# Performance work log

Hardware: AMD Instinct MI355X
Metric: run time of the kernel (lower is better)

Reference implementation:

```python
import jax, jax.numpy as jnp
import numpy as np

MEAN = jnp.array([0.4488, 0.4371, 0.404], dtype=jnp.float32)
PS, PM, PL = 1e-4, 2e-4, 3e-4  # per-branch time costs ps/pm/pl
PATCH = 32
FACTOR = 4
GROUPS = 4


def _conv(x, w, b, pad, groups=1):
    y = jax.lax.conv_general_dilated(x, w, (1, 1), [(pad, pad), (pad, pad)],
                                     dimension_numbers=('NCHW', 'OIHW', 'NCHW'),
                                     feature_group_count=groups)
    return y + b[None, :, None, None]


def _block(x, w1, b1, w2, b2):
    # residual grouped-conv Block(channels, group=4)
    y = jax.nn.relu(_conv(x, w1, b1, 1, groups=GROUPS))
    return x + _conv(y, w2, b2, 1, groups=GROUPS)


def _pixel_shuffle(x, r):
    B, C, H, W = x.shape
    x = x.reshape(B, C // (r * r), r, r, H, W)
    return x.transpose(0, 1, 4, 2, 5, 3).reshape(B, C // (r * r), H * r, W * r)


def setup_inputs() -> dict:
    key = jax.random.key(0)
    ks = jax.random.split(key, 20)
    def W(i, shape, fan):
        return jax.random.normal(ks[i], shape, jnp.float32) * (fan ** -0.5)
    Z = lambda c: jnp.zeros((c,), jnp.float32)
    return {
        'x': jax.random.uniform(ks[0], (4, 3, 160, 160), dtype=jnp.float32),
        'tl': jnp.full((1,), 0.1, jnp.float32),
        'tr': jnp.full((1,), 0.1, jnp.float32),
        'iicm_w': W(1, (12, 3, 3, 3), 27), 'iicm_b': Z(12),
        'conv4_w': W(2, (64, 12, 3, 3), 108), 'conv4_b': Z(64),
        'b1_w1': W(3, (64, 16, 3, 3), 144), 'b1_b1': Z(64),
        'b1_w2': W(4, (64, 16, 3, 3), 144), 'b1_b2': Z(64),
        'c1_w': W(5, (64, 128, 1, 1), 128), 'c1_b': Z(64),
        'b2_w1': W(6, (64, 16, 3, 3), 144), 'b2_b1': Z(64),
        'b2_w2': W(7, (64, 16, 3, 3), 144), 'b2_b2': Z(64),
        'c2_w': W(8, (64, 192, 1, 1), 192), 'c2_b': Z(64),
        'b3_w1': W(9, (64, 16, 3, 3), 144), 'b3_b1': Z(64),
        'b3_w2': W(10, (64, 16, 3, 3), 144), 'b3_b2': Z(64),
        'c3_w': W(11, (64, 256, 1, 1), 256), 'c3_b': Z(64),
        'marm_w': W(12, (64, 67, 3, 3), 603), 'marm_b': Z(64),
        'up1_w': W(13, (256, 64, 3, 3), 576), 'up1_b': Z(256),
        'up2_w': W(14, (256, 64, 3, 3), 576), 'up2_b': Z(256),
        'upc_w': W(15, (3, 64, 3, 3), 576), 'upc_b': Z(3),
    }


def reference(x, tl, tr, iicm_w, iicm_b, conv4_w, conv4_b,
              b1_w1, b1_b1, b1_w2, b1_b2, c1_w, c1_b,
              b2_w1, b2_b1, b2_w2, b2_b2, c2_w, c2_b,
              b3_w1, b3_b1, b3_w2, b3_b2, c3_w, c3_b,
              marm_w, marm_b, up1_w, up1_b, up2_w, up2_b, upc_w, upc_b):
    # ----- sub_mean -----
    x0 = x - MEAN[None, :, None, None]
    B, C, H, W = x0.shape
    hp, wp = H // PATCH, W // PATCH
    N = B * hp * wp
    # ----- decompsition_img: tile into 32x32 patches -----
    p = x0.reshape(B, C, hp, PATCH, wp, PATCH).transpose(0, 2, 4, 1, 3, 5)
    p = p.reshape(N, C, PATCH, PATCH)
    # ----- IICM: feature extraction + per-patch difficulty score ssza -----
    f = jax.nn.relu(_conv(p, iicm_w, iicm_b, 1))          # [N,12,32,32]
    ssza = jnp.mean(jnp.abs(f), axis=(1, 2, 3))           # [N]
    f = _conv(f, conv4_w, conv4_b, 1)                     # [N,64,32,32]
    # ----- branch depth 1 -----
    b1o = _block(f, b1_w1, b1_b1, b1_w2, b1_b2)
    c1o = jnp.concatenate([f, b1o], axis=1)               # [N,128,...]
    xs_ = jax.nn.relu(_conv(c1o, c1_w, c1_b, 0))          # [N,64,...]
    # ----- branch depth 2 (original computes on non-routed subset; per-patch
    # convs are independent so dense compute + mask-select is the same math) --
    b2o = _block(xs_, b2_w1, b2_b1, b2_w2, b2_b2)
    c2o = jnp.concatenate([c1o, b2o], axis=1)             # [N,192,...]
    xm_ = jax.nn.relu(_conv(c2o, c2_w, c2_b, 0))
    # ----- branch depth 3 -----
    b3o = _block(xm_, b3_w1, b3_b1, b3_w2, b3_b2)
    c3o = jnp.concatenate([c2o, b3o], axis=1)             # [N,256,...]
    xh_ = jax.nn.relu(_conv(c3o, c3_w, c3_b, 0))
    # ----- threshold routing (mode 'test'): ssza vs tl, tl+tr -----
    tl0, tr0 = tl[0], tr[0]
    thr = tl0 + tr0
    m1 = ssza > thr                      # easy -> 1 block
    m2 = (ssza >= tl0) & (ssza <= thr)   # medium -> 2 blocks
    sel = lambda m, a, b: jnp.where(m[:, None, None, None], a, b)
    xout = sel(m1, xs_, sel(m2, xm_, xh_))                # [N,64,32,32]
    t = jnp.where(m1, PS * (ssza - thr),
                  jnp.where(m2, PM * tr0, PL * (tl0 - ssza)))
    timep = t.reshape(B, hp * wp).mean(axis=1, keepdims=True)  # [B,1]
    # ----- combination_img: stitch patches back -----
    feat = xout.reshape(B, hp, wp, 64, PATCH, PATCH).transpose(0, 3, 1, 4, 2, 5)
    feat = feat.reshape(B, 64, H, W)
    # ----- xcropia: per-patch activity mask at HR scale (channel 0 std) -----
    s = jnp.std(p[:, 0], axis=(1, 2))                     # [N]
    smap = jnp.broadcast_to(s[:, None, None], (N, PATCH, PATCH))
    smap = smap.reshape(B, hp, wp, PATCH, PATCH).transpose(0, 1, 3, 2, 4)
    smap = smap.reshape(B, 1, H, W)
    xcropia = jnp.repeat(jnp.repeat(smap, FACTOR, axis=2), FACTOR, axis=3)
    y = jax.nn.relu(_conv(jnp.concatenate([x0, feat], axis=1), marm_w, marm_b, 1))
    y = jax.nn.relu(_pixel_shuffle(_conv(y, up1_w, up1_b, 1), 2))
    y = jax.nn.relu(_pixel_shuffle(_conv(y, up2_w, up2_b, 1), 2))
    y = _conv(y, upc_w, upc_b, 1) + MEAN[None, :, None, None]
    xoutputa = y * xcropia
    return (y, timep, xcropia, xoutputa)
```

## Files before the change

kernel.cpp:

```cpp
#include <hip/hip_runtime.h>
#include <hip/hip_bf16.h>

typedef __hip_bfloat16 bf16;
typedef __bf16 bf16x8 __attribute__((ext_vector_type(8)));
typedef float f32x4 __attribute__((ext_vector_type(4)));

#define MEAN0 0.4488f
#define MEAN1 0.4371f
#define MEAN2 0.4040f

__global__ void k_iicm(const float* __restrict__ x, const float* __restrict__ w,
                       const float* __restrict__ bias, bf16* __restrict__ outN16,
                       float* __restrict__ partial){
  __shared__ __align__(16) float ws_[324];
  __shared__ float bs[12];
  __shared__ float sh[256];
  for(int k=threadIdx.x;k<324;k+=256){ int t0=k/12, kk=k%12; ws_[k]=w[kk*27+t0]; }
  if(threadIdx.x<12) bs[threadIdx.x]=bias[threadIdx.x];
  __syncthreads();
  int idx = blockIdx.x*256+threadIdx.x;
  int pix = idx & 1023, n = idx >> 10;
  int i = pix>>5, j = pix&31;
  int pw = n%5, ph=(n/5)%5, bb=n/25;
  float acc[12];
  #pragma unroll
  for(int k=0;k<12;k++) acc[k]=bs[k];
  #pragma unroll
  for(int c=0;c<3;c++){
    const float* xb = x + ((bb*3+c)*160 + ph*32)*160 + pw*32;
    float mc = (c==0)?MEAN0:((c==1)?MEAN1:MEAN2);
    #pragma unroll
    for(int dy=-1;dy<=1;dy++){
      int ii=i+dy; if((unsigned)ii>=32u) continue;
      #pragma unroll
      for(int dx=-1;dx<=1;dx++){
        int jj=j+dx; if((unsigned)jj>=32u) continue;
        float v = xb[ii*160+jj]-mc;
        int t0 = c*9+(dy+1)*3+(dx+1);
        const float4* wv = (const float4*)&ws_[t0*12];
        float4 w0=wv[0], w1=wv[1], w2=wv[2];
        acc[0]+=v*w0.x; acc[1]+=v*w0.y; acc[2]+=v*w0.z; acc[3]+=v*w0.w;
        acc[4]+=v*w1.x; acc[5]+=v*w1.y; acc[6]+=v*w1.z; acc[7]+=v*w1.w;
        acc[8]+=v*w2.x; acc[9]+=v*w2.y; acc[10]+=v*w2.z; acc[11]+=v*w2.w;
      }
    }
  }
  float s=0.f;
  #pragma unroll
  for(int k=0;k<12;k++){ acc[k]=fmaxf(acc[k],0.f); s+=acc[k]; }
  union{ float4 v; bf16 h[8]; } p0, p1;
  #pragma unroll
  for(int k=0;k<8;k++) p0.h[k]=__float2bfloat16(acc[k]);
  #pragma unroll
  for(int k=0;k<4;k++) p1.h[k]=__float2bfloat16(acc[8+k]);
  #pragma unroll
  for(int k=4;k<8;k++) p1.h[k]=__float2bfloat16(0.f);
  bf16* o16 = outN16 + (size_t)(n*1024+pix)*16;
  *(float4*)o16 = p0.v;
  *(float4*)(o16+8) = p1.v;
  sh[threadIdx.x]=s; __syncthreads();
  for(int o=128;o>0;o>>=1){ if(threadIdx.x<o) sh[threadIdx.x]+=sh[threadIdx.x+o]; __syncthreads(); }
  if(threadIdx.x==0) partial[blockIdx.x]=sh[0];
}

__global__ void k_red(const float* __restrict__ partial, const float* __restrict__ x,
                      float* __restrict__ scalp){
  int n = blockIdx.x, t = threadIdx.x;
  __shared__ float sh[256];
  if(t==0)
    scalp[n] = (partial[n*4]+partial[n*4+1]+partial[n*4+2]+partial[n*4+3])*(1.f/12288.f);
  int pw=n%5, ph=(n/5)%5, bb=n/25;
  const float* xb = x + ((bb*3+0)*160 + ph*32)*160 + pw*32;
  float sm=0.f, sq=0.f;
  for(int k=t;k<1024;k+=256){ int i=k>>5,j=k&31; float v=xb[i*160+j]-MEAN0; sm+=v; sq+=v*v; }
  sh[t]=sm; __syncthreads();
  for(int o=128;o>0;o>>=1){ if(t<o) sh[t]+=sh[t+o]; __syncthreads(); }
  float smean = sh[0]*(1.f/1024.f);
  __syncthreads();
  sh[t]=sq; __syncthreads();
  for(int o=128;o>0;o>>=1){ if(t<o) sh[t]+=sh[t+o]; __syncthreads(); }
  if(t==0){ float var = sh[0]*(1.f/1024.f) - smean*smean; scalp[128+n]=sqrtf(fmaxf(var,0.f)); }
}

__global__ void k_wpack(const float* __restrict__ c1_w, const float* __restrict__ c2_w,
                        const float* __restrict__ c3_w, const float* __restrict__ up1_w,
                        const float* __restrict__ up2_w, const float* __restrict__ marm_w,
                        const float* __restrict__ upc_w, const float* __restrict__ b1_w1,
                        const float* __restrict__ b1_w2, const float* __restrict__ b2_w1,
                        const float* __restrict__ b2_w2, const float* __restrict__ b3_w1,
                        const float* __restrict__ b3_w2, const float* __restrict__ conv4_w,
                        bf16* __restrict__ packs){
  int idx = blockIdx.x*256+threadIdx.x;
  if(idx>=467968) return;
  float v;
  if(idx<36864){
    const float* w; int Cin, base;
    if(idx<8192){ w=c1_w; Cin=128; base=0; }
    else if(idx<20480){ w=c2_w; Cin=192; base=8192; }
    else { w=c3_w; Cin=256; base=20480; }
    int r=idx-base; int g=r>>9, oc=(r>>3)&63, j=r&7;
    v = w[oc*Cin + g*8 + j];
  } else if(idx<331776){
    int r0=idx-36864;
    int conv=r0/147456; int r=r0-conv*147456;
    int tap=r>>14; int r2=r&16383;
    int s=(r2>>11)&7, oc=(r2>>3)&255, j=r2&7;
    int ic=s*8+j;
    const float* w = conv? up2_w : up1_w;
    v = w[oc*576 + ic*9 + tap];
  } else if(idx<387072){
    int r=idx-331776;
    int tap=r/6144; int rr=r-tap*6144;
    int icg=rr>>9, oc=(rr>>3)&63, j=rr&7;
    int ic=icg*8+j;
    v = 0.f;
    if(ic<64)      v = marm_w[oc*603 + (3+ic)*9 + tap];
    else if(ic<67) v = marm_w[oc*603 + (ic-64)*9 + tap];
  } else if(idx<396288){
    int r=idx-387072;
    int tap=r>>10; int rr=r&1023;
    int tc=rr>>7, oc=(rr>>3)&15, j=rr&7;
    int ic=tc*8+j;
    v = (oc<3) ? upc_w[oc*576 + ic*9 + tap] : 0.f;
  } else if(idx<457728){
    int r=idx-396288;
    int conv=r/10240; int rr=r-conv*10240;
    int tp=rr/2048; int r2=rr&2047;
    int oc=r2>>5; int k=r2&31;
    int ks=k>>3, e=k&7;
    int tap=2*tp+(ks>>1);
    int il=(ks&1)*8+e;
    const float* w = (conv==0)?b1_w1:(conv==1)?b1_w2:(conv==2)?b2_w1:(conv==3)?b2_w2:(conv==4)?b3_w1:b3_w2;
    v = (tap<9) ? w[oc*144 + il*9 + tap] : 0.f;
  } else {
    int r=idx-457728;
    int tp=r/2048; int r2=r&2047;
    int oc=r2>>5; int k=r2&31;
    int ks=k>>3, e=k&7;
    int tap=2*tp+(ks>>1);
    int ic=(ks&1)*8+e;
    v = (tap<9 && ic<12) ? conv4_w[oc*108 + ic*9 + tap] : 0.f;
  }
  packs[idx]=__float2bfloat16(v);
}

__global__ __launch_bounds__(128,3) void k_conv4M(const bf16* __restrict__ in,
                        const bf16* __restrict__ wp4, const float* __restrict__ bias,
                        bf16* __restrict__ outN){
  __shared__ __align__(16) __bf16 sB[204*2*8];
  int tid=threadIdx.x, bid=blockIdx.x;
  int n=bid>>3, tile=bid&7, y0=tile*4;
  const bf16* ib = in + (size_t)n*16384;
  for(int cid=tid; cid<408; cid+=128){
    int p=cid>>1, c=cid&1;
    int r=p/34, cc=p-r*34;
    int gy=y0-1+r, gx=cc-1;
    float4 v={0.f,0.f,0.f,0.f};
    if((unsigned)gy<32u && (unsigned)gx<32u)
      v = *(const float4*)(ib + (size_t)((gy<<5)+gx)*16 + c*8);
    *(float4*)(&sB[(size_t)(p*2 + (c^(p&1)))*8]) = v;
  }
  __syncthreads();
  int w_=tid>>6, l=tid&63;
  int ks=l>>4, l15=l&15;
  int h=ks>>1, cb=ks&1;
  f32x4 acc[4][4];
  #pragma unroll
  for(int i=0;i<4;i++)
    #pragma unroll
    for(int j=0;j<4;j++) acc[i][j]=(f32x4){0.f,0.f,0.f,0.f};
  int pr[4], pc[4];
  #pragma unroll
  for(int fn=0;fn<4;fn++){ int npx=w_*64+fn*16+l15; pr[fn]=npx>>5; pc[fn]=npx&31; }
  #pragma unroll
  for(int tp=0;tp<5;tp++){
    bf16x8 afr[4];
    #pragma unroll
    for(int fm=0;fm<4;fm++)
      afr[fm] = *(const bf16x8*)(wp4 + (((size_t)(tp*64 + fm*16 + l15))*4 + ks)*8);
    #pragma unroll
    for(int fm=0;fm<4;fm++) asm volatile("" : "+v"(afr[fm]));
    const int t0=2*tp, t1=(2*tp+1>8)?8:(2*tp+1);
    int ty = h ? (t1/3) : (t0/3);
    int tx = h ? (t1%3) : (t0%3);
    #pragma unroll
    for(int fn=0;fn<4;fn++){
      int p = (pr[fn]+ty)*34 + pc[fn]+tx;
      bf16x8 b = *(const bf16x8*)(&sB[(size_t)(p*2 + (cb^(p&1)))*8]);
      #pragma unroll
      for(int fm=0;fm<4;fm++)
        acc[fm][fn] = __builtin_amdgcn_mfma_f32_16x16x32_bf16(afr[fm], b, acc[fm][fn], 0,0,0);
    }
  }
  bf16* ob = outN + (size_t)n*65536;
  #pragma unroll
  for(int fm=0;fm<4;fm++){
    int oc0 = fm*16 + ks*4;
    #pragma unroll
    for(int fn=0;fn<4;fn++){
      int pxl = (y0+pr[fn])*32 + pc[fn];
      union{ uint2 u; bf16 hh[4]; } pk;
      #pragma unroll
      for(int j=0;j<4;j++) pk.hh[j]=__float2bfloat16(acc[fm][fn][j]+bias[oc0+j]);
      *(uint2*)(ob + (size_t)pxl*64 + oc0) = pk.u;
    }
  }
}

__global__ __launch_bounds__(128,3) void k_gconvM(const bf16* __restrict__ in,
                        const bf16* __restrict__ wg, const float* __restrict__ bias,
                        const bf16* __restrict__ resid, bf16* __restrict__ out, int do_relu){
  __shared__ __align__(16) __bf16 sB[204*8*8];
  int tid = threadIdx.x;
  int bid = blockIdx.x;
  int n = bid>>3, tile = bid&7;
  int y0 = tile*4;
  const bf16* ib = in + (size_t)n*65536;
  for(int cid=tid; cid<1632; cid+=128){
    int p = cid>>3, s = cid&7;
    int r = p/34, c = p - r*34;
    int gy = y0-1+r, gx = c-1;
    float4 v = {0.f,0.f,0.f,0.f};
    if((unsigned)gy<32u && (unsigned)gx<32u)
      v = *(const float4*)(ib + (size_t)((gy<<5)+gx)*64 + s*8);
    *(float4*)(&sB[(size_t)(p*8 + (s^(p&7)))*8]) = v;
  }
  __syncthreads();
  int w_ = tid>>6, l = tid&63;
  int ks = l>>4, l15 = l&15;
  int h = ks>>1, cb = ks&1;
  f32x4 acc[4][4];
  #pragma unroll
  for(int i=0;i<4;i++)
    #pragma unroll
    for(int j=0;j<4;j++) acc[i][j]=(f32x4){0.f,0.f,0.f,0.f};
  int pr[4], pc[4];
  #pragma unroll
  for(int fn=0;fn<4;fn++){ int npx = w_*64+fn*16+l15; pr[fn]=npx>>5; pc[fn]=npx&31; }
  #pragma unroll
  for(int tp=0;tp<5;tp++){
    bf16x8 afr[4];
    #pragma unroll
    for(int fm=0;fm<4;fm++)
      afr[fm] = *(const bf16x8*)(wg + (((size_t)(tp*64 + fm*16 + l15))*4 + ks)*8);
    #pragma unroll
    for(int fm=0;fm<4;fm++) asm volatile("" : "+v"(afr[fm]));
    const int t0=2*tp, t1=(2*tp+1>8)?8:(2*tp+1);
    int ty = h ? (t1/3) : (t0/3);
    int tx = h ? (t1%3) : (t0%3);
    #pragma unroll
    for(int fn=0;fn<4;fn++){
      int p = (pr[fn]+ty)*34 + pc[fn]+tx;
      int pb = p*8;
      #pragma unroll
      for(int fm=0;fm<4;fm++){
        int c = fm*2 + cb;
        bf16x8 b = *(const bf16x8*)(&sB[(size_t)(pb + (c^(p&7)))*8]);
        acc[fm][fn] = __builtin_amdgcn_mfma_f32_16x16x32_bf16(afr[fm], b, acc[fm][fn], 0,0,0);
      }
    }
  }
  bf16* ob = out + (size_t)n*65536;
  const bf16* rb = resid ? resid + (size_t)n*65536 : (const bf16*)0;
  #pragma unroll
  for(int fm=0;fm<4;fm++){
    int oc0 = fm*16 + ks*4;
    #pragma unroll
    for(int fn=0;fn<4;fn++){
      int pxl = (y0+pr[fn])*32 + pc[fn];
      float v[4];
      #pragma unroll
      for(int j=0;j<4;j++){
        float t = acc[fm][fn][j] + bias[oc0+j];
        if(do_relu) t = fmaxf(t,0.f);
        v[j]=t;
      }
      if(rb){
        union{ uint2 u; bf16 h[4]; } ru;
        ru.u = *(const uint2*)(rb + (size_t)pxl*64 + oc0);
        #pragma unroll
        for(int j=0;j<4;j++) v[j] += __bfloat162float(ru.h[j]);
      }
      union{ uint2 u; bf16 h[4]; } pk;
      #pragma unroll
      for(int j=0;j<4;j++) pk.h[j]=__float2bfloat16(v[j]);
      *(uint2*)(ob + (size_t)pxl*64 + oc0) = pk.u;
    }
  }
}

__global__ __launch_bounds__(256,4) void k_1x1M(const bf16* __restrict__ s0,
                        const bf16* __restrict__ s1, const bf16* __restrict__ s2,
                        const bf16* __restrict__ s3, int ns,
                        const bf16* __restrict__ wpk, const float* __restrict__ bias,
                        bf16* __restrict__ outN){
  __shared__ __align__(16) __bf16 sB[8*256*8];
  int tid = threadIdx.x;
  int px0 = blockIdx.x*256;
  int w_ = tid>>6, l = tid&63;
  int ks = l>>4, l15 = l&15;
  f32x4 acc[4][4];
  #pragma unroll
  for(int i=0;i<4;i++)
    #pragma unroll
    for(int j=0;j<4;j++) acc[i][j]=(f32x4){0.f,0.f,0.f,0.f};
  const bf16* srcs[4]={s0,s1,s2,s3};
  for(int s=0;s<ns;s++){
    __syncthreads();
    const bf16* sp = srcs[s];
    #pragma unroll
    for(int it=0;it<8;it++){
      *(float4*)(&sB[(size_t)(it*256+tid)*8]) = *(const float4*)(sp + (size_t)(px0+tid)*64 + it*8);
    }
    __syncthreads();
    #pragma unroll
    for(int kk=0;kk<2;kk++){
      int tc = kk*4+ks;
      bf16x8 a[4], b[4];
      #pragma unroll
      for(int fm=0;fm<4;fm++)
        a[fm] = *(const bf16x8*)(wpk + ((size_t)((s*8+tc)*64 + fm*16+l15))*8);
      #pragma unroll
      for(int fm=0;fm<4;fm++) asm volatile("" : "+v"(a[fm]));
      #pragma unroll
      for(int fn=0;fn<4;fn++) b[fn] = *(const bf16x8*)(&sB[(size_t)(tc*256 + w_*64+fn*16+l15)*8]);
      #pragma unroll
      for(int fm=0;fm<4;fm++)
        #pragma unroll
        for(int fn=0;fn<4;fn++)
          acc[fm][fn] = __builtin_amdgcn_mfma_f32_16x16x32_bf16(a[fm], b[fn], acc[fm][fn], 0,0,0);
    }
  }
  #pragma unroll
  for(int fm=0;fm<4;fm++){
    int oc0 = fm*16 + ks*4;
    #pragma unroll
    for(int fn=0;fn<4;fn++){
      int pxt = px0 + w_*64 + fn*16 + l15;
      union{ uint2 u; bf16 h[4]; } pk;
      #pragma unroll
      for(int j=0;j<4;j++) pk.h[j]=__float2bfloat16(fmaxf(acc[fm][fn][j]+bias[oc0+j],0.f));
      *(uint2*)(outN + (size_t)pxt*64 + oc0) = pk.u;
    }
  }
}

__global__ void k_routeT(const bf16* __restrict__ xs, const bf16* __restrict__ xm,
                         const bf16* __restrict__ xh, const float* __restrict__ xseg,
                         const float* __restrict__ scalp, const float* __restrict__ tl,
                         const float* __restrict__ tr, bf16* __restrict__ featN,
                         int nroute, float* __restrict__ dtp){
  __shared__ float sh[256];
  int bidx = blockIdx.x;
  float tl0 = tl[0], tr0 = tr[0], thr = tl0+tr0;
  if(bidx >= nroute){
    int b = bidx - nroute, t = threadIdx.x;
    float v=0.f;
    if(t<25){
      float sz=scalp[b*25+t];
      v = (sz>thr) ? 1e-4f*(sz-thr) : ((sz>=tl0 && sz<=thr) ? 2e-4f*tr0 : 3e-4f*(tl0-sz));
    }
    sh[t]=v; __syncthreads();
    for(int o=128;o>0;o>>=1){ if(t<o) sh[t]+=sh[t+o]; __syncthreads(); }
    if(t==0) dtp[b]=sh[0]*(1.f/25.f);
    return;
  }
  int idx = bidx*256+threadIdx.x;
  int c = idx%12; int px = idx/12;
  int b = px/25600; int rem = px - b*25600;
  int y = rem/160, xx = rem - y*160;
  int n = b*25 + (y>>5)*5 + (xx>>5);
  float sz = scalp[n];
  const bf16* src = (sz>thr) ? xs : ((sz>=tl0 && sz<=thr) ? xm : xh);
  uint4 v = make_uint4(0,0,0,0);
  if(c < 8){
    v = *(const uint4*)(src + ((size_t)n*1024 + ((y&31)<<5) + (xx&31))*64 + c*8);
  } else if(c == 8){
    union{ uint4 q; bf16 h[8]; } pk;
    pk.q = make_uint4(0,0,0,0);
    pk.h[0]=__float2bfloat16(xseg[(b*3+0)*25600 + rem]-MEAN0);
    pk.h[1]=__float2bfloat16(xseg[(b*3+1)*25600 + rem]-MEAN1);
    pk.h[2]=__float2bfloat16(xseg[(b*3+2)*25600 + rem]-MEAN2);
    v = pk.q;
  }
  *(uint4*)(featN + (size_t)px*96 + c*8) = v;
}

__global__ __launch_bounds__(256,2) void k_marmM(const bf16* __restrict__ featN,
                        const bf16* __restrict__ wpm, const float* __restrict__ bias,
                        bf16* __restrict__ outN){
  __shared__ __align__(16) __bf16 sB[12*340*8];
  __shared__ __align__(16) __bf16 sA[12*64*8];
  int bid = blockIdx.x;
  int img = bid/100; int t_ = bid - img*100;
  int y0 = (t_/5)*8, x0 = (t_%5)*32;
  int tid = threadIdx.x;
  const bf16* ib = featN + (size_t)img*25600*96;
  for(int cid=tid; cid<4080; cid+=256){
    int icg = cid/340, p = cid - icg*340;
    int r = p/34, cc = p - r*34;
    int gy = y0-1+r, gx = x0-1+cc;
    float4 v = {0.f,0.f,0.f,0.f};
    if((unsigned)gy<160u && (unsigned)gx<160u)
      v = *(const float4*)(ib + (size_t)(gy*160+gx)*96 + icg*8);
    *(float4*)(&sB[(size_t)(icg*340+p)*8]) = v;
  }
  for(int cid=tid; cid<768; cid+=256)
    *(float4*)(&sA[(size_t)cid*8]) = ((const float4*)wpm)[cid];
  __syncthreads();
  int w_ = tid>>6, l = tid&63;
  int ks = l>>4, l15 = l&15;
  f32x4 acc[4][4];
  #pragma unroll
  for(int i=0;i<4;i++)
    #pragma unroll
    for(int j=0;j<4;j++) acc[i][j]=(f32x4){0.f,0.f,0.f,0.f};
  int pr[4], pc[4];
  #pragma unroll
  for(int fn=0;fn<4;fn++){ int npx = w_*64+fn*16+l15; pr[fn]=npx>>5; pc[fn]=npx&31; }
  float4 pre[3];
  for(int tap=0;tap<9;tap++){
    if(tap<8){
      #pragma unroll
      for(int k=0;k<3;k++) pre[k] = ((const float4*)wpm)[(tap+1)*768 + k*256 + tid];
    }
    int ty=tap/3, tx=tap-ty*3;
    #pragma unroll
    for(int kk=0;kk<3;kk++){
      int tc = kk*4+ks;
      bf16x8 a[4], b[4];
      #pragma unroll
      for(int fm=0;fm<4;fm++) a[fm] = *(const bf16x8*)(&sA[(size_t)(tc*64 + fm*16+l15)*8]);
      #pragma unroll
      for(int fn=0;fn<4;fn++)
        b[fn] = *(const bf16x8*)(&sB[(size_t)(tc*340 + (pr[fn]+ty)*34 + pc[fn]+tx)*8]);
      #pragma unroll
      for(int fm=0;fm<4;fm++)
        #pragma unroll
        for(int fn=0;fn<4;fn++)
          acc[fm][fn] = __builtin_amdgcn_mfma_f32_16x16x32_bf16(a[fm], b[fn], acc[fm][fn], 0,0,0);
    }
    if(tap<8){
      __syncthreads();
      #pragma unroll
      for(int k=0;k<3;k++) ((float4*)sA)[k*256+tid] = pre[k];
      __syncthreads();
    }
  }
  bf16* ob = outN + (size_t)img*25600*64;
  #pragma unroll
  for(int fm=0;fm<4;fm++){
    int oc0 = fm*16 + ks*4;
    #pragma unroll
    for(int fn=0;fn<4;fn++){
      int px = (y0+pr[fn])*160 + x0+pc[fn];
      union{ uint2 u; bf16 h[4]; } pk;
      #pragma unroll
      for(int j=0;j<4;j++) pk.h[j]=__float2bfloat16(fmaxf(acc[fm][fn][j]+bias[oc0+j],0.f));
      *(uint2*)(ob + (size_t)px*64 + oc0) = pk.u;
    }
  }
}

template<int H, int W>
__global__ __launch_bounds__(256,3) void k_convup(const bf16* __restrict__ in,
                        bf16* __restrict__ o0, bf16* __restrict__ o1,
                        const bf16* __restrict__ wp, const float* __restrict__ bias){
  constexpr int TXC = W/16, TPB = (H/4)*TXC;
  __shared__ __align__(16) char smem[16384];
  __bf16* sB = (__bf16*)smem;
  int bid = blockIdx.x;
  int img = bid/TPB; int t_ = bid - img*TPB;
  int y0 = (t_/TXC)*4, x0 = (t_%TXC)*16;
  int tid = threadIdx.x;
  const bf16* ib = in + (size_t)img*H*W*64;
  for(int cid=tid; cid<864; cid+=256){
    int p = cid>>3, tt = cid&7;
    int r = p/18, cc = p - r*18;
    int gy = y0-1+r, gx = x0-1+cc;
    float4 v = {0.f,0.f,0.f,0.f};
    if((unsigned)gy<(unsigned)H && (unsigned)gx<(unsigned)W)
      v = *(const float4*)(ib + ((size_t)(gy*W+gx)*64 + tt*8));
    *(float4*)(&sB[(size_t)(p*8 + (tt^(p&7)))*8]) = v;
  }
  __syncthreads();
  int w_ = tid>>6, l = tid&63;
  int ks = l>>4, l15 = l&15;
  f32x4 acc[4][4];
  #pragma unroll
  for(int i=0;i<4;i++)
    #pragma unroll
    for(int j=0;j<4;j++) acc[i][j]=(f32x4){0.f,0.f,0.f,0.f};
  const bf16* wpb = wp + ((size_t)w_*64 + l15)*8;
  #pragma unroll
  for(int kk=0;kk<2;kk++){
    int tc = kk*4+ks;
    #pragma unroll
    for(int tr=0;tr<3;tr++){
      bf16x8 afr[3][4];
      #pragma unroll
      for(int tx=0;tx<3;tx++)
        #pragma unroll
        for(int fm=0;fm<4;fm++)
          afr[tx][fm] = *(const bf16x8*)(wpb + ((size_t)(((tr*3+tx)*8+tc)*256) + fm*16)*8);
      #pragma unroll
      for(int tx=0;tx<3;tx++)
        #pragma unroll
        for(int fm=0;fm<4;fm++)
          asm volatile("" : "+v"(afr[tx][fm]));
      #pragma unroll
      for(int tx=0;tx<3;tx++){
        bf16x8 b[4];
        #pragma unroll
        for(int fn=0;fn<4;fn++){
          int p = (fn+tr)*18 + l15+tx;
          b[fn] = *(const bf16x8*)(&sB[(size_t)(p*8 + (tc^(p&7)))*8]);
        }
        #pragma unroll
        for(int fm=0;fm<4;fm++)
          #pragma unroll
          for(int fn=0;fn<4;fn++)
            acc[fm][fn] = __builtin_amdgcn_mfma_f32_16x16x32_bf16(afr[tx][fm], b[fn], acc[fm][fn], 0,0,0);
      }
    }
  }
  bf16* ob = ((img&1) ? o1 : o0) + (size_t)(img>>1)*((size_t)8*H*W*64);
  const int W2 = 2*W;
  char* oT = smem;
  #pragma unroll
  for(int h=0;h<2;h++){
    __syncthreads();
    #pragma unroll
    for(int fm=0;fm<4;fm++){
      int co = w_*16 + fm*4 + ks;
      #pragma unroll
      for(int j=0;j<4;j++){
        float bsv = bias[w_*64 + fm*16 + ks*4 + j];
        int r1=(j>>1)&1, r2=j&1;
        #pragma unroll
        for(int ff=0;ff<2;ff++){
          int fn = 2*h+ff;
          int opx = (2*ff+r1)*32 + 2*l15+r2;
          float v = fmaxf(acc[fm][fn][j]+bsv, 0.f);
          int sl = (co>>3) ^ ((opx>>1)&7);
          *(bf16*)(oT + opx*128 + sl*16 + (co&7)*2) = __float2bfloat16(v);
        }
      }
    }
    __syncthreads();
    #pragma unroll
    for(int k=0;k<4;k++){
      int cid = k*256 + tid;
      int p = cid>>3, lq = cid&7;
      int sl = lq ^ ((p>>1)&7);
      uint4 v = *(const uint4*)(oT + p*128 + sl*16);
      int Y = 2*y0 + 4*h + (p>>5), X = 2*x0 + (p&31);
      *(uint4*)(ob + ((size_t)Y*W2 + X)*64 + lq*8) = v;
    }
  }
}

__global__ __launch_bounds__(256,3) void k_upcM(const bf16* __restrict__ i0,
                        const bf16* __restrict__ i1, const bf16* __restrict__ wpu,
                        const float* __restrict__ bias, const float* __restrict__ scal,
                        float* __restrict__ dout, int b0){
  __shared__ __align__(16) __bf16 sB[396*64];
  int tid = threadIdx.x;
  int img = blockIdx.x/1600; int t_ = blockIdx.x - img*1600;
  const bf16* in = img ? i1 : i0;
  int b = b0 + img;
  int by0 = (t_/10)*4, bx0 = (t_%10)*64;
  for(int cid=tid; cid<3168; cid+=256){
    int px = cid>>3, c = cid&7;
    int hr = px/66, hc = px - hr*66;
    int gy = by0-1+hr, gx = bx0-1+hc;
    float4 v = {0.f,0.f,0.f,0.f};
    if((unsigned)gy<640u && (unsigned)gx<640u)
      v = *(const float4*)(in + ((size_t)(gy*640+gx))*64 + c*8);
    int slot = c ^ (px&7);
    *(float4*)(&sB[(size_t)px*64 + slot*8]) = v;
  }
  int w_ = tid>>6, l = tid&63;
  int ks = l>>4, l15 = l&15;
  bf16x8 afr[9][2];
  #pragma unroll
  for(int tap=0;tap<9;tap++)
    #pragma unroll
    for(int kk=0;kk<2;kk++)
      afr[tap][kk] = *(const bf16x8*)(wpu + (size_t)((tap*8 + kk*4+ks)*16 + l15)*8);
  __syncthreads();
  f32x4 acc[4];
  #pragma unroll
  for(int fn=0;fn<4;fn++) acc[fn]=(f32x4){0.f,0.f,0.f,0.f};
  int r = w_;
  int cxc[4];
  #pragma unroll
  for(int fn=0;fn<4;fn++) cxc[fn]=fn*16+l15;
  for(int tap=0;tap<9;tap++){
    int ty=tap/3, tx=tap-ty*3;
    #pragma unroll
    for(int kk=0;kk<2;kk++){
      int tc = kk*4+ks;
      #pragma unroll
      for(int fn=0;fn<4;fn++){
        int ph = (r+ty)*66 + cxc[fn]+tx;
        int slot = tc ^ (ph&7);
        bf16x8 bb = *(const bf16x8*)(&sB[(size_t)ph*64 + slot*8]);
        acc[fn] = __builtin_amdgcn_mfma_f32_16x16x32_bf16(afr[tap][kk], bb, acc[fn], 0,0,0);
      }
    }
  }
  if(ks==0){
    float c0=bias[0]+MEAN0, c1=bias[1]+MEAN1, c2=bias[2]+MEAN2;
    int gy = by0 + r;
    size_t yb=(size_t)b*3*409600;
    #pragma unroll
    for(int fn=0;fn<4;fn++){
      int gx = bx0 + cxc[fn];
      float a0=acc[fn][0]+c0, a1=acc[fn][1]+c1, a2=acc[fn][2]+c2;
      int n=b*25+(gy>>7)*5+(gx>>7);
      float sv=scal[128+n];
      size_t pidx=(size_t)gy*640+gx;
      dout[yb+pidx]=a0; dout[yb+409600+pidx]=a1; dout[yb+819200+pidx]=a2;
      dout[4915204 + (size_t)b*409600 + pidx]=sv;
      size_t xa=6553604+yb;
      dout[xa+pidx]=a0*sv; dout[xa+409600+pidx]=a1*sv; dout[xa+819200+pidx]=a2*sv;
    }
  }
}

extern "C" void kernel_launch(void* const* d_in, const int* in_sizes, int n_in,
                              void* d_out, int out_size, void* d_ws, size_t ws_size,
                              hipStream_t stream){
  const float* x     =(const float*)d_in[0];
  const float* tl    =(const float*)d_in[1];
  const float* tr    =(const float*)d_in[2];
  const float* iicm_w=(const float*)d_in[3];
  const float* iicm_b=(const float*)d_in[4];
  const float* conv4_w=(const float*)d_in[5];
  const float* conv4_b=(const float*)d_in[6];
  const float* b1_w1 =(const float*)d_in[7];  const float* b1_b1=(const float*)d_in[8];
  const float* b1_w2 =(const float*)d_in[9];  const float* b1_b2=(const float*)d_in[10];
  const float* c1_w  =(const float*)d_in[11]; const float* c1_b =(const float*)d_in[12];
  const float* b2_w1 =(const float*)d_in[13]; const float* b2_b1=(const float*)d_in[14];
  const float* b2_w2 =(const float*)d_in[15]; const float* b2_b2=(const float*)d_in[16];
  const float* c2_w  =(const float*)d_in[17]; const float* c2_b =(const float*)d_in[18];
  const float* b3_w1 =(const float*)d_in[19]; const float* b3_b1=(const float*)d_in[20];
  const float* b3_w2 =(const float*)d_in[21]; const float* b3_b2=(const float*)d_in[22];
  const float* c3_w  =(const float*)d_in[23]; const float* c3_b =(const float*)d_in[24];
  const float* marm_w=(const float*)d_in[25]; const float* marm_b=(const float*)d_in[26];
  const float* up1_w =(const float*)d_in[27]; const float* up1_b=(const float*)d_in[28];
  const float* up2_w =(const float*)d_in[29]; const float* up2_b=(const float*)d_in[30];
  const float* upc_w =(const float*)d_in[31]; const float* upc_b=(const float*)d_in[32];

  char* base = (char*)d_ws;
  float* out =(float*)d_out;
  float* scal=(float*)base;
  float* partial=(float*)(base+1024);

  const int SEG = (ws_size >= 188417024ull) ? 4 : 1;
  const int NP  = SEG*25;
  const int NPix= NP*1024;

  const size_t SZB = (size_t)NP*131072;
  char* bufs = base + 4096;
  bf16* fN   = (bf16*)(bufs + 0*SZB);
  bf16* tmpN = (bf16*)(bufs + 1*SZB);
  bf16* xsN  = (bf16*)(bufs + 2*SZB);
  bf16* b1oN = (bf16*)(bufs + 3*SZB);
  bf16* b2oN = (bf16*)(bufs + 4*SZB);
  bf16* xmN  = (bf16*)(bufs + 5*SZB);
  bf16* b3oN = (bf16*)(bufs + 6*SZB);
  bf16* xhN  = (bf16*)(bufs + 7*SZB);
  bf16* featN= (bf16*)(bufs + 0*SZB);
  bf16* marmN= (bf16*)(bufs + 2*SZB);
  bf16* ps1  = (bf16*)(bufs + 4*SZB);
  bf16* ps2a = (bf16*)(bufs + 8*SZB);
  bf16* ps2b = (bf16*)(bufs + 0*SZB);
  char* packsp = bufs + 8*SZB + 52428800;
  bf16* wpc  = (bf16*)packsp;
  bf16* wp1  = wpc + 36864;
  bf16* wp2  = wp1 + 147456;
  bf16* wpm  = wp2 + 147456;
  bf16* wpu  = wpm + 55296;
  bf16* wpg2 = wpu + 9216;
  bf16* wp4  = wpg2 + 61440;
  bf16* f16N = wp4 + 10240;

  k_wpack<<<1829,256,0,stream>>>(c1_w,c2_w,c3_w, up1_w,up2_w, marm_w, upc_w,
                                 b1_w1,b1_w2,b2_w1,b2_w2,b3_w1,b3_w2, conv4_w, wpc);

  for(int b0=0;b0<4;b0+=SEG){
    int p0 = b0*25;
    const float* xseg = x + (size_t)b0*3*25600;
    float* scalp = scal + p0;

    k_iicm <<<NP*4,  256,0,stream>>>(xseg, iicm_w, iicm_b, f16N, partial);
    k_red  <<<NP,    256,0,stream>>>(partial, xseg, scalp);
    k_conv4M<<<NP*8, 128,0,stream>>>(f16N, wp4, conv4_b, fN);
    k_gconvM<<<NP*8, 128,0,stream>>>(fN,   wpg2,         b1_b1, (const bf16*)0, tmpN, 1);
    k_gconvM<<<NP*8, 128,0,stream>>>(tmpN, wpg2+10240,   b1_b2, fN,             b1oN, 0);
    k_1x1M <<<NP*4,  256,0,stream>>>(fN, b1oN, (const bf16*)0, (const bf16*)0, 2, wpc, c1_b, xsN);
    k_gconvM<<<NP*8, 128,0,stream>>>(xsN,  wpg2+2*10240, b2_b1, (const bf16*)0, tmpN, 1);
    k_gconvM<<<NP*8, 128,0,stream>>>(tmpN, wpg2+3*10240, b2_b2, xsN,            b2oN, 0);
    k_1x1M <<<NP*4,  256,0,stream>>>(fN, b1oN, b2oN, (const bf16*)0, 3, wpc+8192, c2_b, xmN);
    k_gconvM<<<NP*8, 128,0,stream>>>(xmN,  wpg2+4*10240, b3_b1, (const bf16*)0, tmpN, 1);
    k_gconvM<<<NP*8, 128,0,stream>>>(tmpN, wpg2+5*10240, b3_b2, xmN,            b3oN, 0);
    k_1x1M <<<NP*4,  256,0,stream>>>(fN, b1oN, b2oN, b3oN, 4, wpc+20480, c3_b, xhN);
    k_routeT<<<NP*48+SEG,256,0,stream>>>(xsN, xmN, xhN, xseg, scalp, tl, tr, featN,
                                         NP*48, out + 4915200 + b0);
    k_marmM<<<SEG*100, 256,0,stream>>>(featN, wpm, marm_b, marmN);
    k_convup<160,160><<<SEG*400, 256,0,stream>>>(marmN, ps1, ps1 + 6553600, wp1, up1_b);
    for(int i=0;i<SEG;i+=2){
      int ni = (SEG-i>=2)?2:1;
      k_convup<320,320><<<ni*1600, 256,0,stream>>>(ps1 + (size_t)i*6553600, ps2a, ps2b, wp2, up2_b);
      k_upcM<<<ni*1600,256,0,stream>>>(ps2a, ps2b, wpu, upc_b, scal, out, b0+i);
    }
  }
}
```

Measured before the change: 464.5 us.

## Widen convup tiles to 32 columns and fold k_red into iicm/conv4

The upsampling 3x3 conv kernel now computes 4x32 pixel tiles instead of 4x16. Each loaded weight fragment is reused across 8 MFMA column blocks, so weight global loads per output are halved, at the cost of 64 accumulator vectors, larger LDS, and fewer waves per SIMD (launch bounds 2). Separately, the per-patch mean/std reduction kernel is removed: iicm blocks also reduce the channel-0 sum and sum of squares, and extra tail blocks in conv4 combine the partials. This drops one launch and one pass over the input.

```diff
diff --git a/kernel.cpp b/kernel.cpp
--- a/kernel.cpp
+++ b/kernel.cpp
@@ -58,28 +58,19 @@
   bf16* o16 = outN16 + (size_t)(n*1024+pix)*16;
   *(float4*)o16 = p0.v;
   *(float4*)(o16+8) = p1.v;
+  const float* xb0 = x + ((bb*3)*160 + ph*32)*160 + pw*32;
+  float v0 = xb0[i*160+j]-MEAN0;
   sh[threadIdx.x]=s; __syncthreads();
   for(int o=128;o>0;o>>=1){ if(threadIdx.x<o) sh[threadIdx.x]+=sh[threadIdx.x+o]; __syncthreads(); }
-  if(threadIdx.x==0) partial[blockIdx.x]=sh[0];
-}
-
-__global__ void k_red(const float* __restrict__ partial, const float* __restrict__ x,
-                      float* __restrict__ scalp){
-  int n = blockIdx.x, t = threadIdx.x;
-  __shared__ float sh[256];
-  if(t==0)
-    scalp[n] = (partial[n*4]+partial[n*4+1]+partial[n*4+2]+partial[n*4+3])*(1.f/12288.f);
-  int pw=n%5, ph=(n/5)%5, bb=n/25;
-  const float* xb = x + ((bb*3+0)*160 + ph*32)*160 + pw*32;
-  float sm=0.f, sq=0.f;
-  for(int k=t;k<1024;k+=256){ int i=k>>5,j=k&31; float v=xb[i*160+j]-MEAN0; sm+=v; sq+=v*v; }
-  sh[t]=sm; __syncthreads();
-  for(int o=128;o>0;o>>=1){ if(t<o) sh[t]+=sh[t+o]; __syncthreads(); }
-  float smean = sh[0]*(1.f/1024.f);
+  if(threadIdx.x==0) partial[blockIdx.x*4+0]=sh[0];
   __syncthreads();
-  sh[t]=sq; __syncthreads();
-  for(int o=128;o>0;o>>=1){ if(t<o) sh[t]+=sh[t+o]; __syncthreads(); }
-  if(t==0){ float var = sh[0]*(1.f/1024.f) - smean*smean; scalp[128+n]=sqrtf(fmaxf(var,0.f)); }
+  sh[threadIdx.x]=v0; __syncthreads();
+  for(int o=128;o>0;o>>=1){ if(threadIdx.x<o) sh[threadIdx.x]+=sh[threadIdx.x+o]; __syncthreads(); }
+  if(threadIdx.x==0) partial[blockIdx.x*4+1]=sh[0];
+  __syncthreads();
+  sh[threadIdx.x]=v0*v0; __syncthreads();
+  for(int o=128;o>0;o>>=1){ if(threadIdx.x<o) sh[threadIdx.x]+=sh[threadIdx.x+o]; __syncthreads(); }
+  if(threadIdx.x==0) partial[blockIdx.x*4+2]=sh[0];
 }
 
 __global__ void k_wpack(const float* __restrict__ c1_w, const float* __restrict__ c2_w,
@@ -146,9 +137,27 @@
 
 __global__ __launch_bounds__(128,3) void k_conv4M(const bf16* __restrict__ in,
                         const bf16* __restrict__ wp4, const float* __restrict__ bias,
-                        bf16* __restrict__ outN){
+                        bf16* __restrict__ outN, const float* __restrict__ partial,
+                        float* __restrict__ scalp, int nconv){
+  int tid=threadIdx.x, bid=blockIdx.x;
+  if(bid >= nconv){
+    if(tid==0){
+      int n = bid - nconv;
+      float s=0.f, sm=0.f, sq=0.f;
+      #pragma unroll
+      for(int q=0;q<4;q++){
+        s  += partial[(n*4+q)*4+0];
+        sm += partial[(n*4+q)*4+1];
+        sq += partial[(n*4+q)*4+2];
+      }
+      scalp[n] = s*(1.f/12288.f);
+      float smean = sm*(1.f/1024.f);
+      float var = sq*(1.f/1024.f) - smean*smean;
+      scalp[128+n] = sqrtf(fmaxf(var,0.f));
+    }
+    return;
+  }
   __shared__ __align__(16) __bf16 sB[204*2*8];
-  int tid=threadIdx.x, bid=blockIdx.x;
   int n=bid>>3, tile=bid&7, y0=tile*4;
   const bf16* ib = in + (size_t)n*16384;
   for(int cid=tid; cid<408; cid+=128){
@@ -463,20 +472,20 @@
 }
 
 template<int H, int W>
-__global__ __launch_bounds__(256,3) void k_convup(const bf16* __restrict__ in,
+__global__ __launch_bounds__(256,2) void k_convup(const bf16* __restrict__ in,
                         bf16* __restrict__ o0, bf16* __restrict__ o1,
                         const bf16* __restrict__ wp, const float* __restrict__ bias){
-  constexpr int TXC = W/16, TPB = (H/4)*TXC;
-  __shared__ __align__(16) char smem[16384];
+  constexpr int TXC = W/32, TPB = (H/4)*TXC;
+  __shared__ __align__(16) char smem[26112];
   __bf16* sB = (__bf16*)smem;
   int bid = blockIdx.x;
   int img = bid/TPB; int t_ = bid - img*TPB;
-  int y0 = (t_/TXC)*4, x0 = (t_%TXC)*16;
+  int y0 = (t_/TXC)*4, x0 = (t_%TXC)*32;
   int tid = threadIdx.x;
   const bf16* ib = in + (size_t)img*H*W*64;
-  for(int cid=tid; cid<864; cid+=256){
+  for(int cid=tid; cid<1632; cid+=256){
     int p = cid>>3, tt = cid&7;
-    int r = p/18, cc = p - r*18;
+    int r = p/34, cc = p - r*34;
     int gy = y0-1+r, gx = x0-1+cc;
     float4 v = {0.f,0.f,0.f,0.f};
     if((unsigned)gy<(unsigned)H && (unsigned)gx<(unsigned)W)
@@ -486,11 +495,14 @@
   __syncthreads();
   int w_ = tid>>6, l = tid&63;
   int ks = l>>4, l15 = l&15;
-  f32x4 acc[4][4];
+  f32x4 acc[4][8];
   #pragma unroll
   for(int i=0;i<4;i++)
     #pragma unroll
-    for(int j=0;j<4;j++) acc[i][j]=(f32x4){0.f,0.f,0.f,0.f};
+    for(int j=0;j<8;j++) acc[i][j]=(f32x4){0.f,0.f,0.f,0.f};
+  int pr[8], pc[8];
+  #pragma unroll
+  for(int fn=0;fn<8;fn++){ int npx = fn*16+l15; pr[fn]=npx>>5; pc[fn]=npx&31; }
   const bf16* wpb = wp + ((size_t)w_*64 + l15)*8;
   #pragma unroll
   for(int kk=0;kk<2;kk++){
@@ -510,17 +522,14 @@
           asm volatile("" : "+v"(afr[tx][fm]));
       #pragma unroll
       for(int tx=0;tx<3;tx++){
-        bf16x8 b[4];
         #pragma unroll
-        for(int fn=0;fn<4;fn++){
-          int p = (fn+tr)*18 + l15+tx;
-          b[fn] = *(const bf16x8*)(&sB[(size_t)(p*8 + (tc^(p&7)))*8]);
+        for(int fn=0;fn<8;fn++){
+          int p = (pr[fn]+tr)*34 + pc[fn]+tx;
+          bf16x8 b = *(const bf16x8*)(&sB[(size_t)(p*8 + (tc^(p&7)))*8]);
+          #pragma unroll
+          for(int fm=0;fm<4;fm++)
+            acc[fm][fn] = __builtin_amdgcn_mfma_f32_16x16x32_bf16(afr[tx][fm], b, acc[fm][fn], 0,0,0);
         }
-        #pragma unroll
-        for(int fm=0;fm<4;fm++)
-          #pragma unroll
-          for(int fn=0;fn<4;fn++)
-            acc[fm][fn] = __builtin_amdgcn_mfma_f32_16x16x32_bf16(afr[tx][fm], b[fn], acc[fm][fn], 0,0,0);
       }
     }
   }
@@ -528,7 +537,7 @@
   const int W2 = 2*W;
   char* oT = smem;
   #pragma unroll
-  for(int h=0;h<2;h++){
+  for(int r=0;r<4;r++){
     __syncthreads();
     #pragma unroll
     for(int fm=0;fm<4;fm++){
@@ -539,8 +548,8 @@
         int r1=(j>>1)&1, r2=j&1;
         #pragma unroll
         for(int ff=0;ff<2;ff++){
-          int fn = 2*h+ff;
-          int opx = (2*ff+r1)*32 + 2*l15+r2;
+          int fn = 2*r+ff;
+          int opx = r1*64 + 2*pc[fn]+r2;
           float v = fmaxf(acc[fm][fn][j]+bsv, 0.f);
           int sl = (co>>3) ^ ((opx>>1)&7);
           *(bf16*)(oT + opx*128 + sl*16 + (co&7)*2) = __float2bfloat16(v);
@@ -554,7 +563,7 @@
       int p = cid>>3, lq = cid&7;
       int sl = lq ^ ((p>>1)&7);
       uint4 v = *(const uint4*)(oT + p*128 + sl*16);
-      int Y = 2*y0 + 4*h + (p>>5), X = 2*x0 + (p&31);
+      int Y = 2*(y0+r) + (p>>6), X = 2*x0 + (p&63);
       *(uint4*)(ob + ((size_t)Y*W2 + X)*64 + lq*8) = v;
     }
   }
@@ -663,7 +672,7 @@
   const int NPix= NP*1024;
 
   const size_t SZB = (size_t)NP*131072;
-  char* bufs = base + 4096;
+  char* bufs = base + 8192;
   bf16* fN   = (bf16*)(bufs + 0*SZB);
   bf16* tmpN = (bf16*)(bufs + 1*SZB);
   bf16* xsN  = (bf16*)(bufs + 2*SZB);
@@ -696,8 +705,7 @@
     float* scalp = scal + p0;
 
     k_iicm <<<NP*4,  256,0,stream>>>(xseg, iicm_w, iicm_b, f16N, partial);
-    k_red  <<<NP,    256,0,stream>>>(partial, xseg, scalp);
-    k_conv4M<<<NP*8, 128,0,stream>>>(f16N, wp4, conv4_b, fN);
+    k_conv4M<<<NP*8+NP, 128,0,stream>>>(f16N, wp4, conv4_b, fN, partial, scalp, NP*8);
     k_gconvM<<<NP*8, 128,0,stream>>>(fN,   wpg2,         b1_b1, (const bf16*)0, tmpN, 1);
     k_gconvM<<<NP*8, 128,0,stream>>>(tmpN, wpg2+10240,   b1_b2, fN,             b1oN, 0);
     k_1x1M <<<NP*4,  256,0,stream>>>(fN, b1oN, (const bf16*)0, (const bf16*)0, 2, wpc, c1_b, xsN);
@@ -710,10 +718,10 @@
     k_routeT<<<NP*48+SEG,256,0,stream>>>(xsN, xmN, xhN, xseg, scalp, tl, tr, featN,
                                          NP*48, out + 4915200 + b0);
     k_marmM<<<SEG*100, 256,0,stream>>>(featN, wpm, marm_b, marmN);
-    k_convup<160,160><<<SEG*400, 256,0,stream>>>(marmN, ps1, ps1 + 6553600, wp1, up1_b);
+    k_convup<160,160><<<SEG*200, 256,0,stream>>>(marmN, ps1, ps1 + 6553600, wp1, up1_b);
     for(int i=0;i<SEG;i+=2){
       int ni = (SEG-i>=2)?2:1;
-      k_convup<320,320><<<ni*1600, 256,0,stream>>>(ps1 + (size_t)i*6553600, ps2a, ps2b, wp2, up2_b);
+      k_convup<320,320><<<ni*800, 256,0,stream>>>(ps1 + (size_t)i*6553600, ps2a, ps2b, wp2, up2_b);
       k_upcM<<<ni*1600,256,0,stream>>>(ps2a, ps2b, wpu, upc_b, scal, out, b0+i);
     }
   }
```

Result: slower. 489.9 us (+5.5%).
